# Kernel tuning notes

Measured on AMD Instinct MI355X. Metric: run time of the kernel, lower is better.

The kernel has to match this reference:

```python
import math
import jax, jax.numpy as jnp
import numpy as np

MODEL_DIM = 4096
NUM_EXPERTS = 64
NUM_TOKENS = 8192
CAPACITY_FACTOR = 1.0


def setup_inputs() -> dict:
    key = jax.random.key(0)
    kx, kw = jax.random.split(key)
    x = jax.random.normal(kx, (NUM_TOKENS, MODEL_DIM), dtype=jnp.float32)
    # nn.Linear weight: [num_experts, model_dim]
    W = jax.random.normal(kw, (NUM_EXPERTS, MODEL_DIM), dtype=jnp.float32) * (1.0 / math.sqrt(MODEL_DIM))
    return {"x": x, "W": W}


def reference(x, W):
    # gating projection (no bias), cast to fp32 as in top1gating
    logits = jnp.matmul(x, W.T).astype(jnp.float32)  # [S, E]
    num_tokens, num_experts = logits.shape
    capacity = int(CAPACITY_FACTOR * math.ceil(num_tokens / num_experts))

    indices1_s = jnp.argmax(logits, axis=1)                        # [S]
    gates = jax.nn.softmax(logits, axis=1)                         # [S, E]
    mask1 = jax.nn.one_hot(indices1_s, num_experts, dtype=jnp.float32)  # [S, E]
    gates1_s = jnp.sum(gates * mask1, axis=1)                      # [S]
    # per-expert running position of each routed token
    locations1 = jnp.cumsum(mask1, axis=0) - 1.0                   # [S, E]
    locations1_s = jnp.sum(locations1 * mask1, axis=1)             # [S]

    return (indices1_s.astype(jnp.int32),
            capacity,
            locations1_s.astype(jnp.int32),
            gates1_s,
            num_experts)
```

## Files before the change

kernel.cpp:

```cpp
#include <hip/hip_runtime.h>
#include <math.h>

#define NTOK 8192
#define MDIM 4096
#define NEXP 64
#define CAPACITY 128.0f

#define OFF_IDX  0
#define OFF_CAP  8192
#define OFF_LOC  8193
#define OFF_GATE 16385
#define OFF_NE   24577

#define NSLICE 16
#define KSL    (MDIM / NSLICE)
#define KC     32
#define NCH    (KSL / KC)

#define WS_CNT_OFF  0
#define WS_RK_OFF   16384
#define WS_PART_OFF 24576

using bf16x8 = __attribute__((ext_vector_type(8))) short;
using f32x4  = __attribute__((ext_vector_type(4))) float;

static __device__ __forceinline__ unsigned short f2bf(float f) {
    union { float f; unsigned u; } v; v.f = f;
    unsigned r = v.u + 0x7fffu + ((v.u >> 16) & 1u);
    return (unsigned short)(r >> 16);
}
static __device__ __forceinline__ float bf2f(unsigned short h) {
    union { unsigned u; float f; } v; v.u = ((unsigned)h) << 16;
    return v.f;
}

__global__ __launch_bounds__(512, 2) void gate_mfma(
    const float* __restrict__ x,
    const float* __restrict__ W,
    float* __restrict__ part)
{
    __shared__ __align__(16) unsigned short wl[NCH * 3][64][32];
    __shared__ __align__(16) float4 xs[8][32][8];

    const int tid   = threadIdx.x;
    const int lane  = tid & 63;
    const int wv    = tid >> 6;
    const int m     = lane & 15;
    const int g     = lane >> 4;
    const int tok0  = blockIdx.x * 256 + wv * 32;
    const int slice = blockIdx.y;
    const int k0    = slice * KSL;

    const float4* __restrict__ x4 = (const float4*)x;

    auto stage = [&](int c) {
        #pragma unroll
        for (int j = 0; j < 4; ++j) {
            const int row  = j * 8 + (lane >> 3);
            const int srcs = (lane & 7) ^ (row & 7);
            const float4* gsrc = x4 + (size_t)(tok0 + row) * (MDIM / 4)
                                 + (k0 >> 2) + c * 8 + srcs;
            void* ldst = (void*)&xs[wv][j * 8][0];
            __builtin_amdgcn_global_load_lds(
                (const __attribute__((address_space(1))) void*)gsrc,
                (__attribute__((address_space(3))) void*)ldst, 16, 0, 0);
        }
    };

    stage(0);

    #pragma unroll
    for (int r = 0; r < 8; ++r) {
        const int j4  = r * 512 + tid;
        const int e   = j4 >> 6;
        const int kk4 = j4 & 63;
        float4 v = *(const float4*)(W + (size_t)e * MDIM + k0 + kk4 * 4);
        const int c    = kk4 >> 3;
        const int slog = (kk4 >> 1) & 3;
        const int half = kk4 & 1;
        const int phys = slog ^ ((e >> 1) & 3);
        float av[4] = {v.x, v.y, v.z, v.w};
        unsigned short h[3][4];
        #pragma unroll
        for (int j = 0; j < 4; ++j) {
            float a = av[j];
            unsigned short b1 = f2bf(a);  float t1 = a  - bf2f(b1);
            unsigned short b2 = f2bf(t1); float t2 = t1 - bf2f(b2);
            unsigned short b3 = f2bf(t2);
            h[0][j] = b1; h[1][j] = b2; h[2][j] = b3;
        }
        #pragma unroll
        for (int t = 0; t < 3; ++t)
            *(ushort4*)&wl[c * 3 + t][e][phys * 8 + half * 4] =
                make_ushort4(h[t][0], h[t][1], h[t][2], h[t][3]);
    }
    __syncthreads();

    auto cvt = [&](float4 lo, float4 hi, bf16x8& r0, bf16x8& r1, bf16x8& r2) {
        float f[8] = {lo.x, lo.y, lo.z, lo.w, hi.x, hi.y, hi.z, hi.w};
        #pragma unroll
        for (int j = 0; j < 8; ++j) {
            float a = f[j];
            unsigned short b1 = f2bf(a);  float t1 = a  - bf2f(b1);
            unsigned short b2 = f2bf(t1); float t2 = t1 - bf2f(b2);
            unsigned short b3 = f2bf(t2);
            r0[j] = (short)b1; r1[j] = (short)b2; r2[j] = (short)b3;
        }
    };

    f32x4 acc[2][4];
    #pragma unroll
    for (int gr = 0; gr < 2; ++gr)
        #pragma unroll
        for (int nt = 0; nt < 4; ++nt) acc[gr][nt] = (f32x4){0.f, 0.f, 0.f, 0.f};

    for (int c = 0; c < NCH; ++c) {
        bf16x8 w[3][4];
        #pragma unroll
        for (int t = 0; t < 3; ++t)
            #pragma unroll
            for (int nt = 0; nt < 4; ++nt) {
                const int e    = nt * 16 + m;
                const int phys = g ^ ((e >> 1) & 3);
                w[t][nt] = *(const bf16x8*)&wl[c * 3 + t][e][phys * 8];
            }

        bf16x8 a[2][3];
        #pragma unroll
        for (int gr = 0; gr < 2; ++gr) {
            const int row = gr * 16 + m;
            float4 lo = xs[wv][row][(2 * g    ) ^ (m & 7)];
            float4 hi = xs[wv][row][(2 * g + 1) ^ (m & 7)];
            cvt(lo, hi, a[gr][0], a[gr][1], a[gr][2]);
        }

        __builtin_amdgcn_sched_barrier(0);
        if (c + 1 < NCH) stage(c + 1);

        #pragma unroll
        for (int gr = 0; gr < 2; ++gr)
            #pragma unroll
            for (int nt = 0; nt < 4; ++nt)
                acc[gr][nt] = __builtin_amdgcn_mfma_f32_16x16x32_bf16(a[gr][2], w[0][nt], acc[gr][nt], 0, 0, 0);
        #pragma unroll
        for (int gr = 0; gr < 2; ++gr)
            #pragma unroll
            for (int nt = 0; nt < 4; ++nt)
                acc[gr][nt] = __builtin_amdgcn_mfma_f32_16x16x32_bf16(a[gr][0], w[2][nt], acc[gr][nt], 0, 0, 0);
        #pragma unroll
        for (int gr = 0; gr < 2; ++gr)
            #pragma unroll
            for (int nt = 0; nt < 4; ++nt)
                acc[gr][nt] = __builtin_amdgcn_mfma_f32_16x16x32_bf16(a[gr][1], w[1][nt], acc[gr][nt], 0, 0, 0);
        #pragma unroll
        for (int gr = 0; gr < 2; ++gr)
            #pragma unroll
            for (int nt = 0; nt < 4; ++nt)
                acc[gr][nt] = __builtin_amdgcn_mfma_f32_16x16x32_bf16(a[gr][1], w[0][nt], acc[gr][nt], 0, 0, 0);
        #pragma unroll
        for (int gr = 0; gr < 2; ++gr)
            #pragma unroll
            for (int nt = 0; nt < 4; ++nt)
                acc[gr][nt] = __builtin_amdgcn_mfma_f32_16x16x32_bf16(a[gr][0], w[1][nt], acc[gr][nt], 0, 0, 0);
        #pragma unroll
        for (int gr = 0; gr < 2; ++gr)
            #pragma unroll
            for (int nt = 0; nt < 4; ++nt)
                acc[gr][nt] = __builtin_amdgcn_mfma_f32_16x16x32_bf16(a[gr][0], w[0][nt], acc[gr][nt], 0, 0, 0);
    }

    #pragma unroll
    for (int gr = 0; gr < 2; ++gr)
        #pragma unroll
        for (int nt = 0; nt < 4; ++nt)
            #pragma unroll
            for (int r = 0; r < 4; ++r) {
                const int tokr = tok0 + gr * 16 + g * 4 + r;
                part[((size_t)slice * NTOK + tokr) * 64 + nt * 16 + m] = acc[gr][nt][r];
            }
}

template<int S>
__global__ __launch_bounds__(256) void reduce_count(
    const float* __restrict__ part,
    float* __restrict__ out,
    int* __restrict__ cnt,
    int* __restrict__ rk)
{
    __shared__ int eidx[32];

    const int tid  = threadIdx.x;
    const int tok0 = blockIdx.x * 32;
    const int trel = tid >> 3;
    const int tok  = tok0 + trel;
    const int q    = tid & 7;

    const float4* __restrict__ p4 = (const float4*)part;

    float4 a[2];
    #pragma unroll
    for (int r = 0; r < 2; ++r) a[r] = make_float4(0.f, 0.f, 0.f, 0.f);
    for (int s = 0; s < S; ++s) {
        #pragma unroll
        for (int r = 0; r < 2; ++r) {
            float4 v = p4[((size_t)s * NTOK + tok) * 16 + q * 2 + r];
            a[r].x += v.x; a[r].y += v.y; a[r].z += v.z; a[r].w += v.w;
        }
    }

    float vals[8] = {a[0].x, a[0].y, a[0].z, a[0].w,
                     a[1].x, a[1].y, a[1].z, a[1].w};

    float bm = vals[0];
    int   be = q * 8;
    #pragma unroll
    for (int j = 1; j < 8; ++j)
        if (vals[j] > bm) { bm = vals[j]; be = q * 8 + j; }
    #pragma unroll
    for (int off = 1; off <= 4; off <<= 1) {
        float om = __shfl_xor(bm, off, 64);
        int   oe = __shfl_xor(be, off, 64);
        if (om > bm || (om == bm && oe < be)) { bm = om; be = oe; }
    }

    float es = 0.f;
    #pragma unroll
    for (int j = 0; j < 8; ++j) es += expf(vals[j] - bm);
    #pragma unroll
    for (int off = 1; off <= 4; off <<= 1)
        es += __shfl_xor(es, off, 64);

    if (q == 0) {
        out[OFF_IDX  + tok] = (float)be;
        out[OFF_GATE + tok] = 1.0f / es;
        eidx[trel] = be;
    }
    __syncthreads();

    if (tid < 64) {
        const int e = (tid < 32) ? eidx[tid] : -1;
        const unsigned long long lt =
            (tid == 0) ? 0ull : ((~0ull) >> (64 - tid));
        unsigned long long mymask = 0;
        int myrk = 0;
        for (int ee = 0; ee < 64; ++ee) {
            unsigned long long mb = __ballot(e == ee);
            if (tid == ee) mymask = mb;
            if (e == ee)   myrk   = (int)__popcll(mb & lt);
        }
        cnt[blockIdx.x * 64 + tid] = (int)__popcll(mymask);
        if (tid < 32) rk[tok0 + tid] = myrk;
    }
    if (tid == 0 && blockIdx.x == 0) {
        out[OFF_CAP] = CAPACITY;
        out[OFF_NE]  = (float)NEXP;
    }
}

__global__ __launch_bounds__(512) void scan_emit(
    const float* __restrict__ idxf,
    const int* __restrict__ cnt,
    const int* __restrict__ rk,
    float* __restrict__ out)
{
    __shared__ int sc[256][64];
    __shared__ int ps[64][8];

    const int tid = threadIdx.x;
    const int e   = tid >> 3;
    const int q   = tid & 7;

    #pragma unroll
    for (int r = 0; r < 32; ++r) sc[0][r * 512 + tid] = cnt[r * 512 + tid];
    __syncthreads();

    {
        int sum = 0;
        #pragma unroll
        for (int j = 0; j < 32; ++j) sum += sc[q * 32 + j][e];
        ps[e][q] = sum;
    }
    __syncthreads();

    {
        int base = 0;
        for (int qq = 0; qq < 8; ++qq) { if (qq < q) base += ps[e][qq]; }
        #pragma unroll
        for (int j = 0; j < 32; ++j) {
            int ch = q * 32 + j;
            int v  = sc[ch][e];
            sc[ch][e] = base;
            base += v;
        }
    }
    __syncthreads();

    #pragma unroll
    for (int r = 0; r < 16; ++r) {
        const int s  = r * 512 + tid;
        const int ee = (int)idxf[s];
        out[OFF_LOC + s] = (float)(sc[s >> 5][ee] + rk[s]);
    }
}

extern "C" void kernel_launch(void* const* d_in, const int* in_sizes, int n_in,
                              void* d_out, int out_size, void* d_ws, size_t ws_size,
                              hipStream_t stream)
{
    const float* x = (const float*)d_in[0];
    const float* W = (const float*)d_in[1];
    float* out = (float*)d_out;

    int*   cnt  = (int*)d_ws + WS_CNT_OFF;
    int*   rk   = (int*)d_ws + WS_RK_OFF;
    float* part = (float*)d_ws + WS_PART_OFF;

    gate_mfma<<<dim3(32, NSLICE), 512, 0, stream>>>(x, W, part);
    reduce_count<NSLICE><<<256, 256, 0, stream>>>(part, out, cnt, rk);
    scan_emit<<<1, 512, 0, stream>>>(out + OFF_IDX, cnt, rk, out);
}
```

Measured before the change: 227.8 us.

## Halve W split LDS footprint, use packed bf16 convert, raise occupancy to 4

The bf16x3 split of W in LDS is now built in two halves of 4 chunks instead of all 8 at once. This halves the weight LDS buffer so four 512-thread blocks can fit per CU (launch bounds 2→4). Software bf16 rounding is replaced by the hardware v_cvt_pk_bf16_f32 instruction, which converts two floats per op. The cost is an extra barrier and W reload pass midway, plus tighter register pressure under the higher occupancy bound.

```diff
diff --git a/kernel.cpp b/kernel.cpp
--- a/kernel.cpp
+++ b/kernel.cpp
@@ -23,23 +23,32 @@
 
 using bf16x8 = __attribute__((ext_vector_type(8))) short;
 using f32x4  = __attribute__((ext_vector_type(4))) float;
-
-static __device__ __forceinline__ unsigned short f2bf(float f) {
-    union { float f; unsigned u; } v; v.f = f;
-    unsigned r = v.u + 0x7fffu + ((v.u >> 16) & 1u);
-    return (unsigned short)(r >> 16);
-}
-static __device__ __forceinline__ float bf2f(unsigned short h) {
-    union { unsigned u; float f; } v; v.u = ((unsigned)h) << 16;
-    return v.f;
-}
-
-__global__ __launch_bounds__(512, 2) void gate_mfma(
+typedef unsigned int u32;
+
+static __device__ __forceinline__ u32 cvtpk(float a0, float a1) {
+    u32 r;
+    asm("v_cvt_pk_bf16_f32 %0, %1, %2" : "=v"(r) : "v"(a0), "v"(a1));
+    return r;
+}
+
+static __device__ __forceinline__ void split2(
+    float a0, float a1, u32& p1, u32& p2, u32& p3)
+{
+    p1 = cvtpk(a0, a1);
+    float t0 = a0 - __uint_as_float(p1 << 16);
+    float t1 = a1 - __uint_as_float(p1 & 0xffff0000u);
+    p2 = cvtpk(t0, t1);
+    float u0 = t0 - __uint_as_float(p2 << 16);
+    float u1 = t1 - __uint_as_float(p2 & 0xffff0000u);
+    p3 = cvtpk(u0, u1);
+}
+
+__global__ __launch_bounds__(512, 4) void gate_mfma(
     const float* __restrict__ x,
     const float* __restrict__ W,
     float* __restrict__ part)
 {
-    __shared__ __align__(16) unsigned short wl[NCH * 3][64][32];
+    __shared__ __align__(16) unsigned short wl[12][64][32];
     __shared__ __align__(16) float4 xs[8][32][8];
 
     const int tid   = threadIdx.x;
@@ -67,106 +76,105 @@
         }
     };
 
+    auto splitW = [&](int h) {
+        #pragma unroll
+        for (int r = 0; r < 4; ++r) {
+            const int j4  = r * 512 + tid;
+            const int e   = j4 >> 5;
+            const int kk4 = j4 & 31;
+            float4 v = *(const float4*)(W + (size_t)e * MDIM + k0 + h * 128 + kk4 * 4);
+            const int c4    = kk4 >> 3;
+            const int slog  = (kk4 >> 1) & 3;
+            const int half16 = kk4 & 1;
+            const int phys  = slog ^ ((e >> 1) & 3);
+            u32 w1a, w2a, w3a, w1b, w2b, w3b;
+            split2(v.x, v.y, w1a, w2a, w3a);
+            split2(v.z, v.w, w1b, w2b, w3b);
+            *(uint2*)&wl[c4 * 3 + 0][e][phys * 8 + half16 * 4] = make_uint2(w1a, w1b);
+            *(uint2*)&wl[c4 * 3 + 1][e][phys * 8 + half16 * 4] = make_uint2(w2a, w2b);
+            *(uint2*)&wl[c4 * 3 + 2][e][phys * 8 + half16 * 4] = make_uint2(w3a, w3b);
+        }
+    };
+
+    auto cvt = [&](float4 lo, float4 hi, bf16x8& r0, bf16x8& r1, bf16x8& r2) {
+        union { u32 u[4]; bf16x8 v; } P1, P2, P3;
+        split2(lo.x, lo.y, P1.u[0], P2.u[0], P3.u[0]);
+        split2(lo.z, lo.w, P1.u[1], P2.u[1], P3.u[1]);
+        split2(hi.x, hi.y, P1.u[2], P2.u[2], P3.u[2]);
+        split2(hi.z, hi.w, P1.u[3], P2.u[3], P3.u[3]);
+        r0 = P1.v; r1 = P2.v; r2 = P3.v;
+    };
+
+    f32x4 acc[2][4];
+    #pragma unroll
+    for (int gr = 0; gr < 2; ++gr)
+        #pragma unroll
+        for (int nt = 0; nt < 4; ++nt) acc[gr][nt] = (f32x4){0.f, 0.f, 0.f, 0.f};
+
     stage(0);
 
-    #pragma unroll
-    for (int r = 0; r < 8; ++r) {
-        const int j4  = r * 512 + tid;
-        const int e   = j4 >> 6;
-        const int kk4 = j4 & 63;
-        float4 v = *(const float4*)(W + (size_t)e * MDIM + k0 + kk4 * 4);
-        const int c    = kk4 >> 3;
-        const int slog = (kk4 >> 1) & 3;
-        const int half = kk4 & 1;
-        const int phys = slog ^ ((e >> 1) & 3);
-        float av[4] = {v.x, v.y, v.z, v.w};
-        unsigned short h[3][4];
-        #pragma unroll
-        for (int j = 0; j < 4; ++j) {
-            float a = av[j];
-            unsigned short b1 = f2bf(a);  float t1 = a  - bf2f(b1);
-            unsigned short b2 = f2bf(t1); float t2 = t1 - bf2f(b2);
-            unsigned short b3 = f2bf(t2);
-            h[0][j] = b1; h[1][j] = b2; h[2][j] = b3;
-        }
-        #pragma unroll
-        for (int t = 0; t < 3; ++t)
-            *(ushort4*)&wl[c * 3 + t][e][phys * 8 + half * 4] =
-                make_ushort4(h[t][0], h[t][1], h[t][2], h[t][3]);
-    }
-    __syncthreads();
-
-    auto cvt = [&](float4 lo, float4 hi, bf16x8& r0, bf16x8& r1, bf16x8& r2) {
-        float f[8] = {lo.x, lo.y, lo.z, lo.w, hi.x, hi.y, hi.z, hi.w};
-        #pragma unroll
-        for (int j = 0; j < 8; ++j) {
-            float a = f[j];
-            unsigned short b1 = f2bf(a);  float t1 = a  - bf2f(b1);
-            unsigned short b2 = f2bf(t1); float t2 = t1 - bf2f(b2);
-            unsigned short b3 = f2bf(t2);
-            r0[j] = (short)b1; r1[j] = (short)b2; r2[j] = (short)b3;
-        }
-    };
-
-    f32x4 acc[2][4];
-    #pragma unroll
-    for (int gr = 0; gr < 2; ++gr)
-        #pragma unroll
-        for (int nt = 0; nt < 4; ++nt) acc[gr][nt] = (f32x4){0.f, 0.f, 0.f, 0.f};
-
-    for (int c = 0; c < NCH; ++c) {
-        bf16x8 w[3][4];
-        #pragma unroll
-        for (int t = 0; t < 3; ++t)
-            #pragma unroll
-            for (int nt = 0; nt < 4; ++nt) {
-                const int e    = nt * 16 + m;
-                const int phys = g ^ ((e >> 1) & 3);
-                w[t][nt] = *(const bf16x8*)&wl[c * 3 + t][e][phys * 8];
+    for (int h = 0; h < 2; ++h) {
+        if (h) __syncthreads();
+        splitW(h);
+        __syncthreads();
+
+        #pragma unroll
+        for (int c4 = 0; c4 < 4; ++c4) {
+            const int c = h * 4 + c4;
+
+            bf16x8 w[3][4];
+            #pragma unroll
+            for (int t = 0; t < 3; ++t)
+                #pragma unroll
+                for (int nt = 0; nt < 4; ++nt) {
+                    const int e    = nt * 16 + m;
+                    const int phys = g ^ ((e >> 1) & 3);
+                    w[t][nt] = *(const bf16x8*)&wl[c4 * 3 + t][e][phys * 8];
+                }
+
+            bf16x8 a[2][3];
+            #pragma unroll
+            for (int gr = 0; gr < 2; ++gr) {
+                const int row = gr * 16 + m;
+                float4 lo = xs[wv][row][(2 * g    ) ^ (m & 7)];
+                float4 hi = xs[wv][row][(2 * g + 1) ^ (m & 7)];
+                cvt(lo, hi, a[gr][0], a[gr][1], a[gr][2]);
             }
 
-        bf16x8 a[2][3];
-        #pragma unroll
-        for (int gr = 0; gr < 2; ++gr) {
-            const int row = gr * 16 + m;
-            float4 lo = xs[wv][row][(2 * g    ) ^ (m & 7)];
-            float4 hi = xs[wv][row][(2 * g + 1) ^ (m & 7)];
-            cvt(lo, hi, a[gr][0], a[gr][1], a[gr][2]);
-        }
-
-        __builtin_amdgcn_sched_barrier(0);
-        if (c + 1 < NCH) stage(c + 1);
-
-        #pragma unroll
-        for (int gr = 0; gr < 2; ++gr)
-            #pragma unroll
-            for (int nt = 0; nt < 4; ++nt)
-                acc[gr][nt] = __builtin_amdgcn_mfma_f32_16x16x32_bf16(a[gr][2], w[0][nt], acc[gr][nt], 0, 0, 0);
-        #pragma unroll
-        for (int gr = 0; gr < 2; ++gr)
-            #pragma unroll
-            for (int nt = 0; nt < 4; ++nt)
-                acc[gr][nt] = __builtin_amdgcn_mfma_f32_16x16x32_bf16(a[gr][0], w[2][nt], acc[gr][nt], 0, 0, 0);
-        #pragma unroll
-        for (int gr = 0; gr < 2; ++gr)
-            #pragma unroll
-            for (int nt = 0; nt < 4; ++nt)
-                acc[gr][nt] = __builtin_amdgcn_mfma_f32_16x16x32_bf16(a[gr][1], w[1][nt], acc[gr][nt], 0, 0, 0);
-        #pragma unroll
-        for (int gr = 0; gr < 2; ++gr)
-            #pragma unroll
-            for (int nt = 0; nt < 4; ++nt)
-                acc[gr][nt] = __builtin_amdgcn_mfma_f32_16x16x32_bf16(a[gr][1], w[0][nt], acc[gr][nt], 0, 0, 0);
-        #pragma unroll
-        for (int gr = 0; gr < 2; ++gr)
-            #pragma unroll
-            for (int nt = 0; nt < 4; ++nt)
-                acc[gr][nt] = __builtin_amdgcn_mfma_f32_16x16x32_bf16(a[gr][0], w[1][nt], acc[gr][nt], 0, 0, 0);
-        #pragma unroll
-        for (int gr = 0; gr < 2; ++gr)
-            #pragma unroll
-            for (int nt = 0; nt < 4; ++nt)
-                acc[gr][nt] = __builtin_amdgcn_mfma_f32_16x16x32_bf16(a[gr][0], w[0][nt], acc[gr][nt], 0, 0, 0);
+            __builtin_amdgcn_sched_barrier(0);
+            if (c + 1 < NCH) stage(c + 1);
+
+            #pragma unroll
+            for (int gr = 0; gr < 2; ++gr)
+                #pragma unroll
+                for (int nt = 0; nt < 4; ++nt)
+                    acc[gr][nt] = __builtin_amdgcn_mfma_f32_16x16x32_bf16(a[gr][2], w[0][nt], acc[gr][nt], 0, 0, 0);
+            #pragma unroll
+            for (int gr = 0; gr < 2; ++gr)
+                #pragma unroll
+                for (int nt = 0; nt < 4; ++nt)
+                    acc[gr][nt] = __builtin_amdgcn_mfma_f32_16x16x32_bf16(a[gr][0], w[2][nt], acc[gr][nt], 0, 0, 0);
+            #pragma unroll
+            for (int gr = 0; gr < 2; ++gr)
+                #pragma unroll
+                for (int nt = 0; nt < 4; ++nt)
+                    acc[gr][nt] = __builtin_amdgcn_mfma_f32_16x16x32_bf16(a[gr][1], w[1][nt], acc[gr][nt], 0, 0, 0);
+            #pragma unroll
+            for (int gr = 0; gr < 2; ++gr)
+                #pragma unroll
+                for (int nt = 0; nt < 4; ++nt)
+                    acc[gr][nt] = __builtin_amdgcn_mfma_f32_16x16x32_bf16(a[gr][1], w[0][nt], acc[gr][nt], 0, 0, 0);
+            #pragma unroll
+            for (int gr = 0; gr < 2; ++gr)
+                #pragma unroll
+                for (int nt = 0; nt < 4; ++nt)
+                    acc[gr][nt] = __builtin_amdgcn_mfma_f32_16x16x32_bf16(a[gr][0], w[1][nt], acc[gr][nt], 0, 0, 0);
+            #pragma unroll
+            for (int gr = 0; gr < 2; ++gr)
+                #pragma unroll
+                for (int nt = 0; nt < 4; ++nt)
+                    acc[gr][nt] = __builtin_amdgcn_mfma_f32_16x16x32_bf16(a[gr][0], w[0][nt], acc[gr][nt], 0, 0, 0);
+        }
     }
 
     #pragma unroll
```

New measurement: 231.5 us. Within noise of the previous version (+1.6%).
